# Performance work log

Measured on AMD Instinct MI355X. Metric: run time of the kernel, lower is better.

Reference implementation:

```python
import jax, jax.numpy as jnp
import numpy as np

B, CIN, COUT, H, W, K = 32, 256, 256, 56, 56, 3
STRIDE, PAD, DIL = 1, 1, 1
SPARSITY = 0.9  # fraction of weight entries pruned to zero


def setup_inputs() -> dict:
    key = jax.random.key(0)
    kx, kw, km = jax.random.split(key, 3)
    x = jax.random.normal(kx, (B, CIN, H, W), dtype=jnp.float32)
    w = jax.random.normal(kw, (COUT, CIN, K, K), dtype=jnp.float32)
    mask = (jax.random.uniform(km, (COUT, CIN, K, K)) > SPARSITY).astype(jnp.float32)
    w = w * mask
    return {"x": x, "weight": w}


def reference(x, weight):
    # Faithful math of SparseConv2D.forward (sparse path == nn.Conv2d, bias=None):
    # NCHW input, OIHW weight, stride/pad/dilation as configured.
    out = jax.lax.conv_general_dilated(
        x, weight,
        window_strides=(STRIDE, STRIDE),
        padding=[(PAD, PAD), (PAD, PAD)],
        rhs_dilation=(DIL, DIL),
        dimension_numbers=("NCHW", "OIHW", "NCHW"),
    )
    return out  # [B, COUT, H_out, W_out]
```

## Files before the change

### kernel.cpp

```cpp
#include <hip/hip_runtime.h>


typedef __attribute__((ext_vector_type(8))) short short8;
typedef __attribute__((ext_vector_type(4))) float f32x4;
typedef __attribute__((ext_vector_type(4))) int i32x4;

constexpr int BB = 32, CIN = 256, COUT = 256, H = 56, W = 56, HW = H * W;
constexpr int HP = 58, WP = 58;

constexpr size_t XP_ELEMS = (size_t)BB * HP * WP * CIN;
constexpr size_t WB_ELEMS = (size_t)COUT * 9 * CIN;
constexpr size_t WS_NEEDED = (XP_ELEMS + WB_ELEMS) * 2;

__device__ __forceinline__ ushort f2bf(float f) {
    unsigned x = __float_as_uint(f);
    unsigned r = (x + 0x7FFFu + ((x >> 16) & 1u)) >> 16;
    return (ushort)r;
}


__global__ __launch_bounds__(256)
void prep_xp(const float* __restrict__ x, ushort* __restrict__ xp) {
    const int bi = blockIdx.x;
    const int b = bi / HP, i = bi % HP;
    ushort* dst = xp + (size_t)bi * WP * CIN;
    const int tid = threadIdx.x;

    if (i == 0 || i == HP - 1) {
        i32x4 z = {0, 0, 0, 0};
        for (int k = tid; k < WP * CIN / 8; k += 256) ((i32x4*)dst)[k] = z;
        return;
    }

    __shared__ ushort t[W][CIN + 2];
    const int lane = tid & 63, wv = tid >> 6;
    if (lane < W) {
        const float* src = x + (size_t)b * CIN * HW + (size_t)(i - 1) * W + lane;
        for (int cin = wv; cin < CIN; cin += 4)
            t[lane][cin] = f2bf(src[(size_t)cin * HW]);
    }
    __syncthreads();
    for (int c = 0; c < WP; ++c)
        dst[c * CIN + tid] = (c == 0 || c == WP - 1) ? (ushort)0 : t[c - 1][tid];
}

__global__ __launch_bounds__(256)
void prep_wb2(const float* __restrict__ w, ushort* __restrict__ wb2) {
    const int d = blockIdx.x * 256 + threadIdx.x;
    const int ci = d & 31;
    const int cout = (d >> 5) & 255;
    const int r = d >> 13;
    const int tap = r % 9, cb = r / 9;
    const int cin = cb * 32 + ci;
    wb2[d] = f2bf(w[((size_t)cout * CIN + cin) * 9 + tap]);
}


#define SCHED_FENCE() __builtin_amdgcn_sched_barrier(0)
#define WAITV0 asm volatile("s_waitcnt vmcnt(0)" ::: "memory")
#define WAITV4 asm volatile("s_waitcnt vmcnt(4)" ::: "memory")
#define WAITV5 asm volatile("s_waitcnt vmcnt(5)" ::: "memory")
#define WAITV6 asm volatile("s_waitcnt vmcnt(6)" ::: "memory")

__device__ __forceinline__ void gload_lds16(const ushort* g, ushort* l) {
    __builtin_amdgcn_global_load_lds(
        (const __attribute__((address_space(1))) void*)g,
        (__attribute__((address_space(3))) void*)l, 16, 0, 0);
}

__device__ __forceinline__ int swz(int c) { return c ^ ((c >> 3) & 7); }

__global__ __launch_bounds__(256, 2)
void conv_mfma(const ushort* __restrict__ xp, const ushort* __restrict__ wb2,
               float* __restrict__ out) {
    int bx = blockIdx.x;
    bx = (bx & 7) * 112 + (bx >> 3);

    const int b  = bx / 28;
    const int p0 = (bx % 28) * 112;
    const int r0 = p0 / 56;

    const int tid  = threadIdx.x;
    const int wv   = tid >> 6;
    const int lane = tid & 63;
    const int ml   = lane & 15;
    const int g    = lane >> 4;

    __shared__ ushort As0[8192], As1[8192];
    __shared__ ushort Xs[8192];

    int aoffB[4];
    #pragma unroll
    for (int mi = 0; mi < 4; ++mi)
        aoffB[mi] = swz((64 * wv + 16 * mi + ml) * 4 + g) * 16;
    int cbase[7];
    #pragma unroll
    for (int nf = 0; nf < 7; ++nf) {
        const int p_  = p0 + 16 * nf + ml;
        const int hl  = (p_ >= p0 + 56) ? 1 : 0;
        const int col = p_ - 56 * (r0 + hl);
        cbase[nf] = hl * 256 + col * 4 + g;
    }
    int goffA[4];
    #pragma unroll
    for (int k = 0; k < 4; ++k) {
        const int c = swz(k * 256 + tid);
        goffA[k] = (c >> 2) * 32 + (c & 3) * 8;
    }
    int xoff;
    {
        const int ii = (tid & 0xC0) | ((tid & 63) ^ (((tid & 63) >> 3) & 7));
        xoff = (ii < 232) ? ((ii >> 2) * CIN + (ii & 3) * 8) : 0;
    }
    const size_t xbase = ((size_t)b * HP + r0) * WP * CIN;

    f32x4 acc[4][7] = {};

    #define STAGE_A(SLAB, BUF)                                                  \
        { const ushort* _s = wb2 + (size_t)(SLAB) * 8192;                       \
          _Pragma("unroll")                                                     \
          for (int k = 0; k < 4; ++k)                                           \
              gload_lds16(_s + goffA[k], &(BUF)[(k * 256 + wv * 64) * 8]); }
    #define STAGE_XROW(RR, CBN)                                                 \
        gload_lds16(xp + xbase + (size_t)(RR) * WP * CIN + (CBN) * 32 + xoff,   \
                    &Xs[((RR) * 256 + wv * 64) * 8])

    STAGE_XROW(0, 0); STAGE_XROW(1, 0); STAGE_XROW(2, 0); STAGE_XROW(3, 0);
    STAGE_A(0, As0);
    STAGE_A(1, As1);
    WAITV0;
    __syncthreads();

    for (int cb = 0; cb < 8; ++cb) {
        const int par = cb & 1;
        const int cbn = (cb < 7) ? cb + 1 : 0;
        #pragma unroll
        for (int tap = 0; tap < 9; ++tap) {
            if      (tap == 0 || tap == 1) { WAITV6; }
            else if (tap == 2 || tap == 5 || tap == 8) { WAITV4; }
            else                            { WAITV5; }
            SCHED_FENCE();
            __builtin_amdgcn_s_barrier();
            SCHED_FENCE();

            const ushort* Ab = (par ^ (tap & 1)) ? As1 : As0;
            const int kh = tap / 3, kw = tap - kh * 3;

            short8 av[4], bv[7];
            #pragma unroll
            for (int mi = 0; mi < 4; ++mi)
                av[mi] = *(const short8*)((const char*)Ab + aoffB[mi]);
            #pragma unroll
            for (int nf = 0; nf < 7; ++nf) {
                const int c = cbase[nf] + kh * 256 + kw * 4;
                bv[nf] = *(const short8*)((const char*)Xs + swz(c) * 16);
            }

            __builtin_amdgcn_s_setprio(1);
            #pragma unroll
            for (int mi = 0; mi < 4; ++mi)
                #pragma unroll
                for (int nf = 0; nf < 7; ++nf)
                    acc[mi][nf] = __builtin_amdgcn_mfma_f32_16x16x32_bf16(
                                      av[mi], bv[nf], acc[mi][nf], 0, 0, 0);
            __builtin_amdgcn_s_setprio(0);
            SCHED_FENCE();
            __builtin_amdgcn_s_barrier();
            SCHED_FENCE();

            {
                int t2 = cb * 9 + tap + 2;
                if (t2 >= 72) t2 -= 72;
                ushort* abuf = (par ^ (tap & 1)) ? As1 : As0;
                STAGE_A(t2, abuf);
            }
            if (tap == 2) { STAGE_XROW(0, cbn); }
            else if (tap == 5) { STAGE_XROW(1, cbn); }
            else if (tap == 8) { STAGE_XROW(2, cbn); STAGE_XROW(3, cbn); }
            SCHED_FENCE();
        }
    }
    WAITV0;

    float* ob = out + (size_t)b * COUT * HW;
    #pragma unroll
    for (int mi = 0; mi < 4; ++mi)
        #pragma unroll
        for (int nf = 0; nf < 7; ++nf)
            #pragma unroll
            for (int r = 0; r < 4; ++r) {
                const int cout_l = 64 * wv + 16 * mi + 4 * g + r;
                const int p_ = p0 + 16 * nf + ml;
                ob[(size_t)cout_l * HW + p_] = acc[mi][nf][r];
            }
    #undef STAGE_A
    #undef STAGE_XROW
}


constexpr int WSZ = CIN * 9;
constexpr int NIN = 54 * 54;

__global__ __launch_bounds__(256)
void sparse_conv3x3(const float* __restrict__ x,
                    const float* __restrict__ wgt,
                    float* __restrict__ out) {
    const int bc = blockIdx.x, cout = bc % COUT, b = bc / COUT;
    const int tid = threadIdx.x;
    __shared__ int2 s_ent[WSZ];
    __shared__ unsigned char s_kk[WSZ];
    __shared__ int s_cnt[257];
    const float* wc = wgt + (size_t)cout * WSZ;
    float mv[9]; int cnt = 0;
    #pragma unroll
    for (int i = 0; i < 9; ++i) { mv[i] = wc[tid * 9 + i]; if (mv[i] != 0.0f) cnt++; }
    s_cnt[tid] = cnt; __syncthreads();
    if (tid == 0) { int run = 0; for (int t = 0; t < 256; ++t) { int c = s_cnt[t]; s_cnt[t] = run; run += c; } s_cnt[256] = run; }
    __syncthreads();
    { int pos = s_cnt[tid];
      #pragma unroll
      for (int i = 0; i < 9; ++i) if (mv[i] != 0.0f) {
          const int kh = i / 3, kw = i - kh * 3;
          int2 e; e.x = (tid * HW + (kh - 1) * W + (kw - 1)) * 4; e.y = __float_as_int(mv[i]);
          s_ent[pos] = e; s_kk[pos] = (unsigned char)(kh | (kw << 4)); pos++; } }
    __syncthreads();
    const int nnz = s_cnt[256];
    const char* xb = (const char*)(x + (size_t)b * CIN * HW);
    float* ob = out + (size_t)bc * HW;
    for (int o = tid; o < HW; o += 256) {
        int h, w; bool interior = (o < NIN);
        if (interior) { h = 1 + o / 54; w = 1 + (o - (h - 1) * 54); }
        else { int o2 = o - NIN;
            if (o2 < 56) { h = 0; w = o2; } else if (o2 < 112) { h = 55; w = o2 - 56; }
            else if (o2 < 166) { h = 1 + (o2 - 112); w = 0; } else { h = 1 + (o2 - 166); w = 55; } }
        const char* pb = xb + (size_t)(h * W + w) * 4;
        float acc = 0.0f;
        if (interior) {
            #pragma unroll 4
            for (int e = 0; e < nnz; ++e) { const int2 en = s_ent[e];
                acc = fmaf(__int_as_float(en.y), *(const float*)(pb + en.x), acc); }
        } else {
            const int h1 = h - 1, w1 = w - 1;
            for (int e = 0; e < nnz; ++e) { const int2 en = s_ent[e]; const int kk = s_kk[e];
                const int hh = h1 + (kk & 15), ww = w1 + (kk >> 4);
                if ((unsigned)hh < (unsigned)H && (unsigned)ww < (unsigned)W)
                    acc = fmaf(__int_as_float(en.y), *(const float*)(pb + en.x), acc); } }
        ob[h * W + w] = acc;
    }
}


extern "C" void kernel_launch(void* const* d_in, const int* in_sizes, int n_in,
                              void* d_out, int out_size, void* d_ws, size_t ws_size,
                              hipStream_t stream) {
    const float* x = (const float*)d_in[0];
    const float* w = (const float*)d_in[1];
    float* out = (float*)d_out;

    if (ws_size >= WS_NEEDED) {
        ushort* xp = (ushort*)d_ws;
        ushort* wbp = xp + XP_ELEMS;
        prep_xp<<<BB * HP, 256, 0, stream>>>(x, xp);
        prep_wb2<<<(int)(WB_ELEMS / 256), 256, 0, stream>>>(w, wbp);
        conv_mfma<<<896, 256, 0, stream>>>(xp, wbp, out);
    } else {
        sparse_conv3x3<<<BB * COUT, 256, 0, stream>>>(x, w, out);
    }
}
```

Baseline: 173.6 us.

## Stage two weight taps per barrier phase to halve barrier count

Restructures the conv main loop so that each barrier-delimited phase covers two filter taps instead of one. The weight LDS buffers are doubled in size so two tap slabs are loaded at once, and input-row staging is done in pairs. The vmcnt waits are retuned to match the new load grouping. This cuts the number of workgroup barriers and waits per channel block. In exchange it raises LDS use, which may lower occupancy from two blocks per CU, and the prefetch distance changes.

```diff
diff --git a/kernel.cpp b/kernel.cpp
--- a/kernel.cpp
+++ b/kernel.cpp
@@ -57,10 +57,7 @@
 
 
 #define SCHED_FENCE() __builtin_amdgcn_sched_barrier(0)
-#define WAITV0 asm volatile("s_waitcnt vmcnt(0)" ::: "memory")
-#define WAITV4 asm volatile("s_waitcnt vmcnt(4)" ::: "memory")
-#define WAITV5 asm volatile("s_waitcnt vmcnt(5)" ::: "memory")
-#define WAITV6 asm volatile("s_waitcnt vmcnt(6)" ::: "memory")
+#define WAITV(N) asm volatile("s_waitcnt vmcnt(" #N ")" ::: "memory")
 
 __device__ __forceinline__ void gload_lds16(const ushort* g, ushort* l) {
     __builtin_amdgcn_global_load_lds(
@@ -86,8 +83,8 @@
     const int ml   = lane & 15;
     const int g    = lane >> 4;
 
-    __shared__ ushort As0[8192], As1[8192];
-    __shared__ ushort Xs[8192];
+    __shared__ ushort As0[2 * 8192], As1[2 * 8192];
+    __shared__ ushort Xs[4 * 2048];
 
     int aoffB[4];
     #pragma unroll
@@ -116,71 +113,100 @@
 
     f32x4 acc[4][7] = {};
 
-    #define STAGE_A(SLAB, BUF)                                                  \
-        { const ushort* _s = wb2 + (size_t)(SLAB) * 8192;                       \
+    #define STAGE_A2(S, BUF)                                                    \
+        { _Pragma("unroll")                                                     \
+          for (int s = 0; s < 2; ++s) {                                         \
+              int _sl = (S) + s; if (_sl >= 72) _sl -= 72;                      \
+              const ushort* _src = wb2 + (size_t)_sl * 8192;                    \
+              _Pragma("unroll")                                                 \
+              for (int k = 0; k < 4; ++k)                                       \
+                  gload_lds16(_src + goffA[k],                                  \
+                              (BUF) + s * 8192 + (k * 256 + wv * 64) * 8);      \
+          } }
+    #define STAGE_A1(S, BUF)                                                    \
+        { int _sl = (S); if (_sl >= 72) _sl -= 72;                              \
+          const ushort* _src = wb2 + (size_t)_sl * 8192;                        \
           _Pragma("unroll")                                                     \
           for (int k = 0; k < 4; ++k)                                           \
-              gload_lds16(_s + goffA[k], &(BUF)[(k * 256 + wv * 64) * 8]); }
-    #define STAGE_XROW(RR, CBN)                                                 \
-        gload_lds16(xp + xbase + (size_t)(RR) * WP * CIN + (CBN) * 32 + xoff,   \
-                    &Xs[((RR) * 256 + wv * 64) * 8])
-
-    STAGE_XROW(0, 0); STAGE_XROW(1, 0); STAGE_XROW(2, 0); STAGE_XROW(3, 0);
-    STAGE_A(0, As0);
-    STAGE_A(1, As1);
-    WAITV0;
-    __syncthreads();
-
-    for (int cb = 0; cb < 8; ++cb) {
-        const int par = cb & 1;
-        const int cbn = (cb < 7) ? cb + 1 : 0;
+              gload_lds16(_src + goffA[k], (BUF) + (k * 256 + wv * 64) * 8); }
+    #define STAGE_XPAIR(RR, CBN)                                                \
+        { _Pragma("unroll")                                                     \
+          for (int r_ = 0; r_ < 2; ++r_)                                        \
+              gload_lds16(xp + xbase + (size_t)((RR) + r_) * WP * CIN           \
+                              + (CBN) * 32 + xoff,                              \
+                          &Xs[(((RR) + r_) * 256 + wv * 64) * 8]); }
+
+    STAGE_XPAIR(0, 0);
+    STAGE_XPAIR(2, 0);
+    STAGE_A2(0, As0);
+    STAGE_A2(2, As1);
+    WAITV(0);
+    __syncthreads();
+
+    #define PHASE(CB, Q, NTAPS, HWAIT)                                          \
+        {                                                                       \
+            WAITV(HWAIT);                                                       \
+            SCHED_FENCE();                                                      \
+            __builtin_amdgcn_s_barrier();                                       \
+            SCHED_FENCE();                                                      \
+            const ushort* Ab = (((CB) + (Q)) & 1) ? As1 : As0;                  \
+            _Pragma("unroll")                                                   \
+            for (int tp = 0; tp < (NTAPS); ++tp) {                              \
+                const int tap = 2 * (Q) + tp;                                   \
+                const int kh = tap / 3, kw = tap - kh * 3;                      \
+                short8 av[4], bv[7];                                            \
+                _Pragma("unroll")                                               \
+                for (int mi = 0; mi < 4; ++mi)                                  \
+                    av[mi] = *(const short8*)((const char*)Ab + tp * 16384      \
+                                              + aoffB[mi]);                     \
+                _Pragma("unroll")                                               \
+                for (int nf = 0; nf < 7; ++nf) {                                \
+                    const int c = cbase[nf] + kh * 256 + kw * 4;                \
+                    bv[nf] = *(const short8*)((const char*)Xs + swz(c) * 16);   \
+                }                                                               \
+                __builtin_amdgcn_s_setprio(1);                                  \
+                _Pragma("unroll")                                               \
+                for (int mi = 0; mi < 4; ++mi)                                  \
+                    _Pragma("unroll")                                           \
+                    for (int nf = 0; nf < 7; ++nf)                              \
+                        acc[mi][nf] = __builtin_amdgcn_mfma_f32_16x16x32_bf16(  \
+                                          av[mi], bv[nf], acc[mi][nf], 0, 0, 0);\
+                __builtin_amdgcn_s_setprio(0);                                  \
+            }                                                                   \
+            SCHED_FENCE();                                                      \
+            __builtin_amdgcn_s_barrier();                                       \
+            SCHED_FENCE();                                                      \
+        }
+
+    for (int cbp = 0; cbp < 4; ++cbp) {
         #pragma unroll
-        for (int tap = 0; tap < 9; ++tap) {
-            if      (tap == 0 || tap == 1) { WAITV6; }
-            else if (tap == 2 || tap == 5 || tap == 8) { WAITV4; }
-            else                            { WAITV5; }
-            SCHED_FENCE();
-            __builtin_amdgcn_s_barrier();
-            SCHED_FENCE();
-
-            const ushort* Ab = (par ^ (tap & 1)) ? As1 : As0;
-            const int kh = tap / 3, kw = tap - kh * 3;
-
-            short8 av[4], bv[7];
-            #pragma unroll
-            for (int mi = 0; mi < 4; ++mi)
-                av[mi] = *(const short8*)((const char*)Ab + aoffB[mi]);
-            #pragma unroll
-            for (int nf = 0; nf < 7; ++nf) {
-                const int c = cbase[nf] + kh * 256 + kw * 4;
-                bv[nf] = *(const short8*)((const char*)Xs + swz(c) * 16);
-            }
-
-            __builtin_amdgcn_s_setprio(1);
-            #pragma unroll
-            for (int mi = 0; mi < 4; ++mi)
-                #pragma unroll
-                for (int nf = 0; nf < 7; ++nf)
-                    acc[mi][nf] = __builtin_amdgcn_mfma_f32_16x16x32_bf16(
-                                      av[mi], bv[nf], acc[mi][nf], 0, 0, 0);
-            __builtin_amdgcn_s_setprio(0);
-            SCHED_FENCE();
-            __builtin_amdgcn_s_barrier();
-            SCHED_FENCE();
-
-            {
-                int t2 = cb * 9 + tap + 2;
-                if (t2 >= 72) t2 -= 72;
-                ushort* abuf = (par ^ (tap & 1)) ? As1 : As0;
-                STAGE_A(t2, abuf);
-            }
-            if (tap == 2) { STAGE_XROW(0, cbn); }
-            else if (tap == 5) { STAGE_XROW(1, cbn); }
-            else if (tap == 8) { STAGE_XROW(2, cbn); STAGE_XROW(3, cbn); }
+        for (int hf = 0; hf < 2; ++hf) {
+            const int cb  = 2 * cbp + hf;
+            const int t0  = 9 * cb;
+            const int cbn = (cb < 7) ? cb + 1 : 0;
+            ushort* bufE = ((cb & 1) == 0) ? As0 : As1;
+            ushort* bufO = ((cb & 1) == 0) ? As1 : As0;
+
+            PHASE(cb, 0, 2, 10);
+            STAGE_A2(t0 + 4, bufE);
+            SCHED_FENCE();
+            PHASE(cb, 1, 2, 8);
+            STAGE_A2(t0 + 6, bufO);
+            SCHED_FENCE();
+            PHASE(cb, 2, 2, 8);
+            STAGE_XPAIR(0, cbn);
+            STAGE_A1(t0 + 8, bufE);
+            SCHED_FENCE();
+            PHASE(cb, 3, 2, 6);
+            STAGE_A2(t0 + 9, bufO);
+            SCHED_FENCE();
+            PHASE(cb, 4, 1, 8);
+            STAGE_XPAIR(2, cbn);
+            STAGE_A2(t0 + 11, bufE);
             SCHED_FENCE();
         }
     }
-    WAITV0;
+    WAITV(0);
 
     float* ob = out + (size_t)b * COUT * HW;
     #pragma unroll
@@ -193,8 +219,10 @@
                 const int p_ = p0 + 16 * nf + ml;
                 ob[(size_t)cout_l * HW + p_] = acc[mi][nf][r];
             }
-    #undef STAGE_A
-    #undef STAGE_XROW
+    #undef STAGE_A2
+    #undef STAGE_A1
+    #undef STAGE_XPAIR
+    #undef PHASE
 }
 
 
```

After: 150.6 us. 13.3% less time.
